# Kernel tuning notes

Hardware: AMD Instinct MI355X
Metric: run time of the kernel (lower is better)

The kernel has to match this reference:

```python
import jax, jax.numpy as jnp
import numpy as np

E = 8          # num_experts
D = 768        # d_model
H = 3072       # d_hidden
TOP_K = 2


def setup_inputs() -> dict:
    key = jax.random.key(0)
    ks = jax.random.split(key, 8)
    s_in = 1.0 / np.sqrt(D)
    s_h = 1.0 / np.sqrt(H)
    return {
        "hidden_states": jax.random.normal(ks[0], (2, 2048, D), dtype=jnp.float32),
        "gate_w": jax.random.normal(ks[1], (E, D), dtype=jnp.float32) * s_in,
        "gate_b": jnp.zeros((E,), dtype=jnp.float32),
        "w1": jax.random.normal(ks[2], (E, H, D), dtype=jnp.float32) * s_in,  # FMoELinear: [E, out, in]
        "b1": jnp.zeros((E, H), dtype=jnp.float32),
        "w2": jax.random.normal(ks[3], (E, D, H), dtype=jnp.float32) * s_h,
        "b2": jnp.zeros((E, D), dtype=jnp.float32),
        "bias": jnp.zeros((D,), dtype=jnp.float32),
    }


def reference(hidden_states, gate_w, gate_b, w1, b1, w2, b2, bias):
    B, S, d = hidden_states.shape
    x = hidden_states.reshape(-1, d)                      # [T, D]
    T = x.shape[0]
    # NaiveGate: linear gate, top-k, softmax over the top-k logits
    logits = x @ gate_w.T + gate_b                        # [T, E]
    top_val, top_idx = jax.lax.top_k(logits, TOP_K)       # [T, K]
    scores = jax.nn.softmax(top_val, axis=-1)             # [T, K]
    # combine weights: [T, E], score mass scattered to chosen experts
    combine = jnp.zeros((T, E), dtype=x.dtype)
    combine = combine.at[jnp.arange(T)[:, None], top_idx].add(scores)
    # expert MLPs (dense over experts, masked combine keeps routing math exact)
    h = jnp.einsum('td,ehd->teh', x, w1) + b1             # [T, E, H]
    h = jax.nn.gelu(h, approximate=False)                 # torch F.gelu (exact erf)
    y = jnp.einsum('teh,edh->ted', h, w2) + b2            # [T, E, D]
    out = jnp.einsum('te,ted->td', combine, y)            # [T, D]
    return out.reshape(B, S, d), bias
```

## Files before the change

### kernel.cpp

```cpp
#include <hip/hip_runtime.h>
#include <hip/hip_bf16.h>

#define DD 768
#define HH 3072
#define NE 8
#define TOPK 2

#define BK 64
#define NB1 (HH / 128)
#define NB2 (DD / 128)
#define SK2 2

typedef __attribute__((ext_vector_type(8))) short short8;
typedef __attribute__((ext_vector_type(4))) float f32x4;

static __device__ __forceinline__ unsigned short f2bf(float v) {
    __hip_bfloat16 b = __float2bfloat16(v);
    return *reinterpret_cast<unsigned short*>(&b);
}

static __device__ __forceinline__ float gelu_f(float v) {
    float s = v * 0.70710678118f;
    float a = fabsf(s);
    float t = __builtin_amdgcn_rcpf(1.f + 0.3275911f * a);
    float poly = t * (0.254829592f + t * (-0.284496736f + t * (1.421413741f +
                 t * (-1.453152027f + t * 1.061405429f))));
    float erfv = 1.f - poly * __expf(-s * s);
    erfv = copysignf(erfv, s);
    return 0.5f * v * (1.f + erfv);
}

__global__ __launch_bounds__(256) void convert_kernel(
    const float* __restrict__ w1, const float* __restrict__ w2,
    unsigned short* __restrict__ w1b, unsigned short* __restrict__ w2b, size_t n)
{
    size_t tid = (size_t)blockIdx.x * blockDim.x + threadIdx.x;
    size_t stride = (size_t)gridDim.x * blockDim.x;
    size_t quarter = n / 4;
    size_t tot = 2 * quarter;
    for (size_t j = tid; j < tot; j += stride) {
        const float* src; unsigned short* dst; size_t off;
        if (j < quarter) { src = w1; dst = w1b; off = j * 4; }
        else             { src = w2; dst = w2b; off = (j - quarter) * 4; }
        float4 v = *reinterpret_cast<const float4*>(&src[off]);
        ushort4 o;
        o.x = f2bf(v.x); o.y = f2bf(v.y); o.z = f2bf(v.z); o.w = f2bf(v.w);
        *reinterpret_cast<ushort4*>(&dst[off]) = o;
    }
}

__global__ __launch_bounds__(256) void init_kernel(int* token_map, int* ctrl, int* qcur, int maxP)
{
    int i = blockIdx.x * blockDim.x + threadIdx.x;
    if (i < maxP) token_map[i] = -1;
    if (i < 64) ctrl[i] = 0;
    if (i < 256) qcur[i] = 0;
}

__global__ __launch_bounds__(256) void gate_kernel(
    const float* __restrict__ x, const float* __restrict__ gw, const float* __restrict__ gb,
    int* __restrict__ topk_idx, float* __restrict__ topk_w, int* __restrict__ ctrl, int T)
{
    __shared__ int hist[NE];
    int tid = threadIdx.x;
    if (tid < NE) hist[tid] = 0;
    __syncthreads();

    int w = tid >> 6, lane = tid & 63;
    for (int t = blockIdx.x * 4 + w; t < T; t += gridDim.x * 4) {
        float acc[NE];
#pragma unroll
        for (int e = 0; e < NE; ++e) acc[e] = 0.f;
        const float4* xr = reinterpret_cast<const float4*>(x + (size_t)t * DD);
        for (int d = lane; d < DD / 4; d += 64) {
            float4 xv = xr[d];
#pragma unroll
            for (int e = 0; e < NE; ++e) {
                float4 gv = *reinterpret_cast<const float4*>(&gw[e * DD + 4 * d]);
                acc[e] += xv.x * gv.x + xv.y * gv.y + xv.z * gv.z + xv.w * gv.w;
            }
        }
#pragma unroll
        for (int e = 0; e < NE; ++e) {
            float v = acc[e];
            for (int off = 32; off; off >>= 1) v += __shfl_xor(v, off, 64);
            acc[e] = v;
        }
        if (lane == 0) {
            float lg[NE];
#pragma unroll
            for (int e = 0; e < NE; ++e) lg[e] = acc[e] + gb[e];
            int i0 = 0;
#pragma unroll
            for (int e = 1; e < NE; ++e) if (lg[e] > lg[i0]) i0 = e;
            int i1 = -1;
#pragma unroll
            for (int e = 0; e < NE; ++e) {
                if (e == i0) continue;
                if (i1 < 0 || lg[e] > lg[i1]) i1 = e;
            }
            float m = lg[i0];
            float e0 = __expf(lg[i0] - m), e1 = __expf(lg[i1] - m);
            float s = e0 + e1;
            topk_idx[2 * t]     = i0;
            topk_idx[2 * t + 1] = i1;
            topk_w[2 * t]       = e0 / s;
            topk_w[2 * t + 1]   = e1 / s;
            atomicAdd(&hist[i0], 1);
            atomicAdd(&hist[i1], 1);
        }
    }
    __syncthreads();
    if (tid < NE && hist[tid] > 0) atomicAdd(&ctrl[tid], hist[tid]);
}

__global__ void offsets_kernel(int* ctrl, int* wq1, int* wq2)
{
    if (threadIdx.x == 0 && blockIdx.x == 0) {
        int nrbs[NE];
        int acc = 0;
        for (int e = 0; e < NE; ++e) {
            ctrl[16 + e] = acc;
            int nrb = (ctrl[e] + 127) >> 7;
            nrbs[e] = nrb;
            acc += nrb << 7;
        }
        ctrl[24] = acc;
        int qc[8], qcum[8];
        for (int q = 0; q < 8; ++q) { qc[q] = 0; qcum[q] = 0; }
        for (int pair = 0; pair < NE * NB1; ++pair) {
            int e = pair / NB1;
            int q = pair & 7;
            int s = qc[q]++;
            qcum[q] += nrbs[e];
            wq1[(q * 24 + s) * 2 + 0] = pair;
            wq1[(q * 24 + s) * 2 + 1] = qcum[q];
        }
        for (int q = 0; q < 8; ++q) { qc[q] = 0; qcum[q] = 0; }
        for (int g = 0; g < NE * NB2 * SK2; ++g) {
            int e = g / (NB2 * SK2);
            int q = g & 7;
            int s = qc[q]++;
            qcum[q] += nrbs[e];
            wq2[(q * 12 + s) * 2 + 0] = g;
            wq2[(q * 12 + s) * 2 + 1] = qcum[q];
        }
    }
}

__global__ __launch_bounds__(256) void scatter_kernel(
    const int* __restrict__ topk_idx, const float* __restrict__ topk_w,
    int* ctrl, int* token_map, int* pos_of, float* wpos, int nA)
{
    __shared__ int lh[NE], lbase[NE];
    int tid = threadIdx.x;
    if (tid < NE) lh[tid] = 0;
    __syncthreads();

    int a = blockIdx.x * blockDim.x + tid;
    int e = 0, rank = 0;
    bool valid = (a < nA);
    if (valid) {
        e = topk_idx[a];
        rank = atomicAdd(&lh[e], 1);
    }
    __syncthreads();
    if (tid < NE && lh[tid] > 0)
        lbase[tid] = atomicAdd(&ctrl[8 + tid], lh[tid]);
    __syncthreads();
    if (valid) {
        int p = ctrl[16 + e] + lbase[e] + rank;
        token_map[p] = a;
        pos_of[a] = p;
        wpos[p] = topk_w[a];
    }
}

__global__ __launch_bounds__(256) void gather_kernel(
    const float* __restrict__ x, const int* __restrict__ token_map,
    unsigned short* __restrict__ Xe, int maxP)
{
    int i = blockIdx.x * blockDim.x + threadIdx.x;
    int total = maxP * (DD / 4);
    if (i >= total) return;
    int r = i / (DD / 4);
    int c = (i % (DD / 4)) * 4;
    int a = token_map[r];
    ushort4 o;
    if (a < 0) {
        o.x = o.y = o.z = o.w = 0;
    } else {
        float4 v = *reinterpret_cast<const float4*>(&x[(size_t)(a >> 1) * DD + c]);
        o.x = f2bf(v.x); o.y = f2bf(v.y); o.z = f2bf(v.z); o.w = f2bf(v.w);
    }
    *reinterpret_cast<ushort4*>(&Xe[(size_t)r * DD + c]) = o;
}

static __device__ __forceinline__ void stage_tile(
    const unsigned short* __restrict__ g, int ld, unsigned short* __restrict__ lds)
{
    int tid = threadIdx.x;
#pragma unroll
    for (int r = 0; r < 4; ++r) {
        int j = (r << 8) + tid;
        int row = j >> 3;
        int kc = (j & 7) ^ (row & 7);
        __builtin_amdgcn_global_load_lds(
            (const __attribute__((address_space(1))) void*)(g + (size_t)row * ld + (kc << 3)),
            (__attribute__((address_space(3))) void*)(lds + (j << 3)),
            16, 0, 0);
    }
}

#define LDSF(base, row, kc) \
    reinterpret_cast<const short8*>(&(base)[((((row) << 3) + ((kc) ^ ((row) & 7))) << 3)])

static __device__ __forceinline__ void gemm_item(
    const unsigned short* __restrict__ Abase,
    const unsigned short* __restrict__ Bbase,
    int ld, int nt,
    unsigned short* __restrict__ As, unsigned short* __restrict__ Bs,
    f32x4 acc[4][4], int wr, int wc, int fr, int fq)
{
    const int BUF = 128 * 64;
    stage_tile(Abase, ld, As);
    stage_tile(Bbase, ld, Bs);
    for (int t = 0; t < nt; ++t) {
        int cur = t & 1;
        if (t + 1 < nt) {
            stage_tile(Abase + (size_t)(t + 1) * BK, ld, As + (cur ^ 1) * BUF);
            stage_tile(Bbase + (size_t)(t + 1) * BK, ld, Bs + (cur ^ 1) * BUF);
            asm volatile("s_waitcnt vmcnt(8)" ::: "memory");
        } else {
            asm volatile("s_waitcnt vmcnt(0)" ::: "memory");
        }
        __builtin_amdgcn_s_barrier();
        asm volatile("" ::: "memory");

        const unsigned short* A = As + cur * BUF;
        const unsigned short* B = Bs + cur * BUF;
        short8 a[2][4], b[2][4];
#pragma unroll
        for (int ks = 0; ks < 2; ++ks) {
            int kc = ks * 4 + fq;
#pragma unroll
            for (int m = 0; m < 4; ++m)
                a[ks][m] = *LDSF(A, wr + m * 16 + fr, kc);
#pragma unroll
            for (int n = 0; n < 4; ++n)
                b[ks][n] = *LDSF(B, wc + n * 16 + fr, kc);
        }
        __builtin_amdgcn_s_setprio(1);
#pragma unroll
        for (int ks = 0; ks < 2; ++ks)
#pragma unroll
            for (int m = 0; m < 4; ++m)
#pragma unroll
                for (int n = 0; n < 4; ++n)
                    acc[m][n] = __builtin_amdgcn_mfma_f32_16x16x32_bf16(
                        b[ks][n], a[ks][m], acc[m][n], 0, 0, 0);
        __builtin_amdgcn_s_setprio(0);
        asm volatile("s_waitcnt lgkmcnt(0)" ::: "memory");
        __builtin_amdgcn_s_barrier();
        asm volatile("" ::: "memory");
    }
}


__global__ __launch_bounds__(256, 2) void gemm1_kernel(
    const unsigned short* __restrict__ Xe, const unsigned short* __restrict__ W1b,
    const float* __restrict__ b1, unsigned short* __restrict__ H1,
    const int* __restrict__ ctrl, const int* __restrict__ wq1, int* __restrict__ qcur)
{
    __shared__ unsigned short As[2 * 128 * 64];
    __shared__ unsigned short Bs[2 * 128 * 64];
    __shared__ int sh_item;
    __shared__ int seg[9];
    __shared__ int tpair[192], tcum[192];

    int tid = threadIdx.x;
    if (tid < 9) seg[tid] = ctrl[16 + tid];
    if (tid < 192) { tpair[tid] = wq1[2 * tid]; tcum[tid] = wq1[2 * tid + 1]; }
    __syncthreads();

    int lane = tid & 63, w = tid >> 6;
    int wr = (w >> 1) * 64, wc = (w & 1) * 64;
    int fr = lane & 15, fq = lane >> 4;
    int q0 = blockIdx.x & 7;

    for (int off = 0; off < 8; ++off) {
        int qq = (q0 + off) & 7;
        int qtot = tcum[qq * 24 + 23];
        for (;;) {
            if (tid == 0) sh_item = atomicAdd(&qcur[qq * 16], 1);
            __syncthreads();
            int j = sh_item;
            __syncthreads();
            if (j >= qtot) break;

            int s = 0;
            while (tcum[qq * 24 + s] <= j) ++s;
            int pair = tpair[qq * 24 + s];
            int start = s ? tcum[qq * 24 + s - 1] : 0;
            int rb = j - start;
            int e = pair / NB1, cb = pair - e * NB1;
            int rowbase = seg[e] + (rb << 7);
            int colbase = cb << 7;

            const unsigned short* Abase = Xe + (size_t)rowbase * DD;
            const unsigned short* Bbase = W1b + (size_t)e * HH * DD + (size_t)colbase * DD;

            f32x4 acc[4][4];
#pragma unroll
            for (int m = 0; m < 4; ++m)
#pragma unroll
                for (int n = 0; n < 4; ++n) acc[m][n] = (f32x4){0.f, 0.f, 0.f, 0.f};

            gemm_item(Abase, Bbase, DD, DD / BK, As, Bs, acc, wr, wc, fr, fq);

            float4 bb[4];
#pragma unroll
            for (int n = 0; n < 4; ++n)
                bb[n] = *reinterpret_cast<const float4*>(
                    &b1[e * HH + colbase + wc + n * 16 + fq * 4]);
#pragma unroll
            for (int m = 0; m < 4; ++m) {
                int tok = rowbase + wr + m * 16 + fr;
#pragma unroll
                for (int n = 0; n < 4; ++n) {
                    int ch = colbase + wc + n * 16 + fq * 4;
                    ushort4 o;
                    o.x = f2bf(gelu_f(acc[m][n][0] + bb[n].x));
                    o.y = f2bf(gelu_f(acc[m][n][1] + bb[n].y));
                    o.z = f2bf(gelu_f(acc[m][n][2] + bb[n].z));
                    o.w = f2bf(gelu_f(acc[m][n][3] + bb[n].w));
                    *reinterpret_cast<ushort4*>(&H1[(size_t)tok * HH + ch]) = o;
                }
            }
        }
    }
}

__global__ __launch_bounds__(256, 2) void gemm2_kernel(
    const unsigned short* __restrict__ H1, const unsigned short* __restrict__ W2b,
    const float* __restrict__ b2, const float* __restrict__ wpos,
    float* __restrict__ Yb, const int* __restrict__ ctrl,
    const int* __restrict__ wq2, int* __restrict__ qcur, int maxP)
{
    __shared__ unsigned short As[2 * 128 * 64];
    __shared__ unsigned short Bs[2 * 128 * 64];
    __shared__ int sh_item;
    __shared__ int seg[9];
    __shared__ int tpair[96], tcum[96];

    int tid = threadIdx.x;
    if (tid < 9) seg[tid] = ctrl[16 + tid];
    if (tid < 96) { tpair[tid] = wq2[2 * tid]; tcum[tid] = wq2[2 * tid + 1]; }
    __syncthreads();

    int lane = tid & 63, w = tid >> 6;
    int wr = (w >> 1) * 64, wc = (w & 1) * 64;
    int fr = lane & 15, fq = lane >> 4;
    int q0 = blockIdx.x & 7;
    size_t Ysz = (size_t)maxP * DD;

    for (int off = 0; off < 8; ++off) {
        int qq = (q0 + off) & 7;
        int qtot = tcum[qq * 12 + 11];
        for (;;) {
            if (tid == 0) sh_item = atomicAdd(&qcur[(8 + qq) * 16], 1);
            __syncthreads();
            int j = sh_item;
            __syncthreads();
            if (j >= qtot) break;

            int s = 0;
            while (tcum[qq * 12 + s] <= j) ++s;
            int g = tpair[qq * 12 + s];
            int start = s ? tcum[qq * 12 + s - 1] : 0;
            int rb = j - start;
            int e = g / (NB2 * SK2);
            int rem = g - e * (NB2 * SK2);
            int cb = rem >> 1;
            int sk = rem & 1;
            int rowbase = seg[e] + (rb << 7);
            int colbase = cb << 7;

            const unsigned short* Abase = H1 + (size_t)rowbase * HH + sk * (HH / 2);
            const unsigned short* Bbase = W2b + (size_t)e * DD * HH + (size_t)colbase * HH + sk * (HH / 2);

            f32x4 acc[4][4];
#pragma unroll
            for (int m = 0; m < 4; ++m)
#pragma unroll
                for (int n = 0; n < 4; ++n) acc[m][n] = (f32x4){0.f, 0.f, 0.f, 0.f};

            gemm_item(Abase, Bbase, HH, HH / BK / SK2, As, Bs, acc, wr, wc, fr, fq);

            float* Yp = Yb + (size_t)sk * Ysz;
            float4 bb[4];
#pragma unroll
            for (int n = 0; n < 4; ++n) {
                float4 b4 = *reinterpret_cast<const float4*>(
                    &b2[e * DD + colbase + wc + n * 16 + fq * 4]);
                bb[n].x = 0.5f * b4.x; bb[n].y = 0.5f * b4.y;
                bb[n].z = 0.5f * b4.z; bb[n].w = 0.5f * b4.w;
            }
#pragma unroll
            for (int m = 0; m < 4; ++m) {
                int tok = rowbase + wr + m * 16 + fr;
                float wp = wpos[tok];
#pragma unroll
                for (int n = 0; n < 4; ++n) {
                    int ch = colbase + wc + n * 16 + fq * 4;
                    float4 o;
                    o.x = wp * (acc[m][n][0] + bb[n].x);
                    o.y = wp * (acc[m][n][1] + bb[n].y);
                    o.z = wp * (acc[m][n][2] + bb[n].z);
                    o.w = wp * (acc[m][n][3] + bb[n].w);
                    *reinterpret_cast<float4*>(&Yp[(size_t)tok * DD + ch]) = o;
                }
            }
        }
    }
}

__global__ __launch_bounds__(256) void combine_kernel(
    const float* __restrict__ Yb, const int* __restrict__ pos_of,
    const float* __restrict__ bias, float* __restrict__ out, int T, int maxP)
{
    int i = blockIdx.x * blockDim.x + threadIdx.x;
    int total = T * (DD / 4);
    size_t Ysz = (size_t)maxP * DD;
    if (i < total) {
        int t = i / (DD / 4);
        int c = (i % (DD / 4)) * 4;
        int p0 = pos_of[2 * t], p1 = pos_of[2 * t + 1];
        float4 v00 = *reinterpret_cast<const float4*>(&Yb[(size_t)p0 * DD + c]);
        float4 v01 = *reinterpret_cast<const float4*>(&Yb[Ysz + (size_t)p0 * DD + c]);
        float4 v10 = *reinterpret_cast<const float4*>(&Yb[(size_t)p1 * DD + c]);
        float4 v11 = *reinterpret_cast<const float4*>(&Yb[Ysz + (size_t)p1 * DD + c]);
        float4 o;
        o.x = v00.x + v01.x + v10.x + v11.x;
        o.y = v00.y + v01.y + v10.y + v11.y;
        o.z = v00.z + v01.z + v10.z + v11.z;
        o.w = v00.w + v01.w + v10.w + v11.w;
        *reinterpret_cast<float4*>(&out[(size_t)t * DD + c]) = o;
    } else if (i < total + DD / 4) {
        int c = (i - total) * 4;
        *reinterpret_cast<float4*>(&out[(size_t)T * DD + c]) =
            *reinterpret_cast<const float4*>(&bias[c]);
    }
}

extern "C" void kernel_launch(void* const* d_in, const int* in_sizes, int n_in,
                              void* d_out, int out_size, void* d_ws, size_t ws_size,
                              hipStream_t stream)
{
    const float* x    = (const float*)d_in[0];
    const float* gw   = (const float*)d_in[1];
    const float* gb   = (const float*)d_in[2];
    const float* w1   = (const float*)d_in[3];
    const float* b1   = (const float*)d_in[4];
    const float* w2   = (const float*)d_in[5];
    const float* b2   = (const float*)d_in[6];
    const float* bias = (const float*)d_in[7];
    float* out = (float*)d_out;

    int T = in_sizes[0] / DD;
    int nA = T * TOPK;
    int maxP = nA + NE * 128;

    char* ws = (char*)d_ws;
    size_t off = 0;
    auto alloc = [&](size_t bytes) -> char* {
        char* p = ws + off;
        off += (bytes + 255) & ~(size_t)255;
        return p;
    };
    unsigned short* w1b = (unsigned short*)alloc((size_t)NE * HH * DD * 2);
    unsigned short* w2b = (unsigned short*)alloc((size_t)NE * DD * HH * 2);
    unsigned short* Xe  = (unsigned short*)alloc((size_t)maxP * DD * 2);
    unsigned short* H1  = (unsigned short*)alloc((size_t)maxP * HH * 2);
    float*  Yb          = (float*)alloc((size_t)SK2 * maxP * DD * 4);
    int*    topk_idx    = (int*)alloc((size_t)nA * 4);
    float*  topk_w      = (float*)alloc((size_t)nA * 4);
    int*    pos_of      = (int*)alloc((size_t)nA * 4);
    float*  wpos        = (float*)alloc((size_t)maxP * 4);
    int*    token_map   = (int*)alloc((size_t)maxP * 4);
    int*    ctrl        = (int*)alloc(64 * 4);
    int*    wq1         = (int*)alloc(384 * 4);
    int*    wq2         = (int*)alloc(192 * 4);
    int*    qcur        = (int*)alloc(256 * 4);

    size_t nW = (size_t)NE * HH * DD;

    hipLaunchKernelGGL(convert_kernel, dim3(4096), dim3(256), 0, stream,
                       w1, w2, w1b, w2b, nW);
    hipLaunchKernelGGL(init_kernel, dim3((maxP + 255) / 256), dim3(256), 0, stream,
                       token_map, ctrl, qcur, maxP);
    hipLaunchKernelGGL(gate_kernel, dim3(512), dim3(256), 0, stream,
                       x, gw, gb, topk_idx, topk_w, ctrl, T);
    hipLaunchKernelGGL(offsets_kernel, dim3(1), dim3(64), 0, stream, ctrl, wq1, wq2);
    hipLaunchKernelGGL(scatter_kernel, dim3((nA + 255) / 256), dim3(256), 0, stream,
                       topk_idx, topk_w, ctrl, token_map, pos_of, wpos, nA);
    hipLaunchKernelGGL(gather_kernel, dim3((maxP * (DD / 4) + 255) / 256), dim3(256), 0, stream,
                       x, token_map, Xe, maxP);
    hipLaunchKernelGGL(gemm1_kernel, dim3(512), dim3(256), 0, stream,
                       Xe, w1b, b1, H1, ctrl, wq1, qcur);
    hipLaunchKernelGGL(gemm2_kernel, dim3(512), dim3(256), 0, stream,
                       H1, w2b, b2, wpos, Yb, ctrl, wq2, qcur, maxP);
    hipLaunchKernelGGL(combine_kernel, dim3((T * (DD / 4) + DD / 4 + 255) / 256, 1, 1), dim3(256), 0, stream,
                       Yb, pos_of, bias, out, T, maxP);
}
```

Baseline: 254.2 us.

## Fuse routing stages into a cooperative kernel and drop split-K in expert GEMM2

The gate, offsets, scatter and gather kernels are merged into one cooperative route kernel that uses grid-wide syncs. The init kernel is folded into the weight-convert kernel, and the token_map/padding zero-fill is removed. GEMM2 no longer splits K in two, which halves the Yb buffer and lets combine read two partial rows instead of four. The aim is fewer launches and less intermediate traffic, at the cost of about half as many GEMM2 work items, lower parallelism, and padding rows of Xe left uninitialised.

```diff
diff --git a/kernel.cpp b/kernel.cpp
--- a/kernel.cpp
+++ b/kernel.cpp
@@ -1,5 +1,8 @@
 #include <hip/hip_runtime.h>
 #include <hip/hip_bf16.h>
+#include <hip/hip_cooperative_groups.h>
+
+namespace cg = cooperative_groups;
 
 #define DD 768
 #define HH 3072
@@ -9,7 +12,6 @@
 #define BK 64
 #define NB1 (HH / 128)
 #define NB2 (DD / 128)
-#define SK2 2
 
 typedef __attribute__((ext_vector_type(8))) short short8;
 typedef __attribute__((ext_vector_type(4))) float f32x4;
@@ -32,9 +34,12 @@
 
 __global__ __launch_bounds__(256) void convert_kernel(
     const float* __restrict__ w1, const float* __restrict__ w2,
-    unsigned short* __restrict__ w1b, unsigned short* __restrict__ w2b, size_t n)
+    unsigned short* __restrict__ w1b, unsigned short* __restrict__ w2b,
+    int* __restrict__ ctrl, int* __restrict__ qcur, size_t n)
 {
     size_t tid = (size_t)blockIdx.x * blockDim.x + threadIdx.x;
+    if (tid < 64) ctrl[tid] = 0;
+    if (tid < 256) qcur[tid] = 0;
     size_t stride = (size_t)gridDim.x * blockDim.x;
     size_t quarter = n / 4;
     size_t tot = 2 * quarter;
@@ -49,79 +54,78 @@
     }
 }
 
-__global__ __launch_bounds__(256) void init_kernel(int* token_map, int* ctrl, int* qcur, int maxP)
-{
-    int i = blockIdx.x * blockDim.x + threadIdx.x;
-    if (i < maxP) token_map[i] = -1;
-    if (i < 64) ctrl[i] = 0;
-    if (i < 256) qcur[i] = 0;
-}
-
-__global__ __launch_bounds__(256) void gate_kernel(
+__global__ __launch_bounds__(256) void route_kernel(
     const float* __restrict__ x, const float* __restrict__ gw, const float* __restrict__ gb,
-    int* __restrict__ topk_idx, float* __restrict__ topk_w, int* __restrict__ ctrl, int T)
-{
+    int* __restrict__ topk_idx, float* __restrict__ topk_w_unused, int* __restrict__ ctrl,
+    int* __restrict__ wq1, int* __restrict__ wq2,
+    int* __restrict__ pos_of, float* __restrict__ wpos, float* __restrict__ topk_w,
+    unsigned short* __restrict__ Xe, int T, int nA)
+{
+    cg::grid_group grid = cg::this_grid();
+    int tid = threadIdx.x, bid = blockIdx.x, nb = gridDim.x;
+    int gidx = bid * 256 + tid;
+
     __shared__ int hist[NE];
-    int tid = threadIdx.x;
     if (tid < NE) hist[tid] = 0;
     __syncthreads();
-
-    int w = tid >> 6, lane = tid & 63;
-    for (int t = blockIdx.x * 4 + w; t < T; t += gridDim.x * 4) {
-        float acc[NE];
-#pragma unroll
-        for (int e = 0; e < NE; ++e) acc[e] = 0.f;
-        const float4* xr = reinterpret_cast<const float4*>(x + (size_t)t * DD);
-        for (int d = lane; d < DD / 4; d += 64) {
-            float4 xv = xr[d];
+    {
+        int w = tid >> 6, lane = tid & 63;
+        for (int t = bid * 4 + w; t < T; t += nb * 4) {
+            float acc[NE];
+#pragma unroll
+            for (int e = 0; e < NE; ++e) acc[e] = 0.f;
+            const float4* xr = reinterpret_cast<const float4*>(x + (size_t)t * DD);
+            for (int d = lane; d < DD / 4; d += 64) {
+                float4 xv = xr[d];
+#pragma unroll
+                for (int e = 0; e < NE; ++e) {
+                    float4 gv = *reinterpret_cast<const float4*>(&gw[e * DD + 4 * d]);
+                    acc[e] += xv.x * gv.x + xv.y * gv.y + xv.z * gv.z + xv.w * gv.w;
+                }
+            }
 #pragma unroll
             for (int e = 0; e < NE; ++e) {
-                float4 gv = *reinterpret_cast<const float4*>(&gw[e * DD + 4 * d]);
-                acc[e] += xv.x * gv.x + xv.y * gv.y + xv.z * gv.z + xv.w * gv.w;
-            }
-        }
-#pragma unroll
-        for (int e = 0; e < NE; ++e) {
-            float v = acc[e];
-            for (int off = 32; off; off >>= 1) v += __shfl_xor(v, off, 64);
-            acc[e] = v;
-        }
-        if (lane == 0) {
-            float lg[NE];
-#pragma unroll
-            for (int e = 0; e < NE; ++e) lg[e] = acc[e] + gb[e];
-            int i0 = 0;
-#pragma unroll
-            for (int e = 1; e < NE; ++e) if (lg[e] > lg[i0]) i0 = e;
-            int i1 = -1;
-#pragma unroll
-            for (int e = 0; e < NE; ++e) {
-                if (e == i0) continue;
-                if (i1 < 0 || lg[e] > lg[i1]) i1 = e;
-            }
-            float m = lg[i0];
-            float e0 = __expf(lg[i0] - m), e1 = __expf(lg[i1] - m);
-            float s = e0 + e1;
-            topk_idx[2 * t]     = i0;
-            topk_idx[2 * t + 1] = i1;
-            topk_w[2 * t]       = e0 / s;
-            topk_w[2 * t + 1]   = e1 / s;
-            atomicAdd(&hist[i0], 1);
-            atomicAdd(&hist[i1], 1);
+                float v = acc[e];
+                for (int off = 32; off; off >>= 1) v += __shfl_xor(v, off, 64);
+                acc[e] = v;
+            }
+            if (lane == 0) {
+                float lg[NE];
+#pragma unroll
+                for (int e = 0; e < NE; ++e) lg[e] = acc[e] + gb[e];
+                int i0 = 0;
+#pragma unroll
+                for (int e = 1; e < NE; ++e) if (lg[e] > lg[i0]) i0 = e;
+                int i1 = -1;
+#pragma unroll
+                for (int e = 0; e < NE; ++e) {
+                    if (e == i0) continue;
+                    if (i1 < 0 || lg[e] > lg[i1]) i1 = e;
+                }
+                float m = lg[i0];
+                float e0 = __expf(lg[i0] - m), e1 = __expf(lg[i1] - m);
+                float s = e0 + e1;
+                topk_idx[2 * t]     = i0;
+                topk_idx[2 * t + 1] = i1;
+                topk_w[2 * t]       = e0 / s;
+                topk_w[2 * t + 1]   = e1 / s;
+                atomicAdd(&hist[i0], 1);
+                atomicAdd(&hist[i1], 1);
+            }
         }
     }
     __syncthreads();
     if (tid < NE && hist[tid] > 0) atomicAdd(&ctrl[tid], hist[tid]);
-}
-
-__global__ void offsets_kernel(int* ctrl, int* wq1, int* wq2)
-{
-    if (threadIdx.x == 0 && blockIdx.x == 0) {
+    __threadfence();
+    grid.sync();
+
+    if (bid == 0 && tid == 0) {
         int nrbs[NE];
         int acc = 0;
         for (int e = 0; e < NE; ++e) {
             ctrl[16 + e] = acc;
-            int nrb = (ctrl[e] + 127) >> 7;
+            int cnt = atomicAdd(&ctrl[e], 0);
+            int nrb = (cnt + 127) >> 7;
             nrbs[e] = nrb;
             acc += nrb << 7;
         }
@@ -137,63 +141,57 @@
             wq1[(q * 24 + s) * 2 + 1] = qcum[q];
         }
         for (int q = 0; q < 8; ++q) { qc[q] = 0; qcum[q] = 0; }
-        for (int g = 0; g < NE * NB2 * SK2; ++g) {
-            int e = g / (NB2 * SK2);
+        for (int g = 0; g < NE * NB2; ++g) {
+            int e = g / NB2;
             int q = g & 7;
             int s = qc[q]++;
             qcum[q] += nrbs[e];
-            wq2[(q * 12 + s) * 2 + 0] = g;
-            wq2[(q * 12 + s) * 2 + 1] = qcum[q];
-        }
-    }
-}
-
-__global__ __launch_bounds__(256) void scatter_kernel(
-    const int* __restrict__ topk_idx, const float* __restrict__ topk_w,
-    int* ctrl, int* token_map, int* pos_of, float* wpos, int nA)
-{
-    __shared__ int lh[NE], lbase[NE];
-    int tid = threadIdx.x;
-    if (tid < NE) lh[tid] = 0;
-    __syncthreads();
-
-    int a = blockIdx.x * blockDim.x + tid;
-    int e = 0, rank = 0;
-    bool valid = (a < nA);
-    if (valid) {
-        e = topk_idx[a];
-        rank = atomicAdd(&lh[e], 1);
-    }
-    __syncthreads();
-    if (tid < NE && lh[tid] > 0)
-        lbase[tid] = atomicAdd(&ctrl[8 + tid], lh[tid]);
-    __syncthreads();
-    if (valid) {
-        int p = ctrl[16 + e] + lbase[e] + rank;
-        token_map[p] = a;
-        pos_of[a] = p;
-        wpos[p] = topk_w[a];
-    }
-}
-
-__global__ __launch_bounds__(256) void gather_kernel(
-    const float* __restrict__ x, const int* __restrict__ token_map,
-    unsigned short* __restrict__ Xe, int maxP)
-{
-    int i = blockIdx.x * blockDim.x + threadIdx.x;
-    int total = maxP * (DD / 4);
-    if (i >= total) return;
-    int r = i / (DD / 4);
-    int c = (i % (DD / 4)) * 4;
-    int a = token_map[r];
-    ushort4 o;
-    if (a < 0) {
-        o.x = o.y = o.z = o.w = 0;
-    } else {
-        float4 v = *reinterpret_cast<const float4*>(&x[(size_t)(a >> 1) * DD + c]);
-        o.x = f2bf(v.x); o.y = f2bf(v.y); o.z = f2bf(v.z); o.w = f2bf(v.w);
-    }
-    *reinterpret_cast<ushort4*>(&Xe[(size_t)r * DD + c]) = o;
+            wq2[(q * 6 + s) * 2 + 0] = g;
+            wq2[(q * 6 + s) * 2 + 1] = qcum[q];
+        }
+        __threadfence();
+    }
+    grid.sync();
+
+    {
+        __shared__ int lh[NE], lbase[NE];
+        for (int a0 = 0; a0 < nA; a0 += nb * 256) {
+            if (tid < NE) lh[tid] = 0;
+            __syncthreads();
+            int a = a0 + gidx;
+            int e = 0, rank = 0;
+            bool valid = (a < nA);
+            if (valid) {
+                e = topk_idx[a];
+                rank = atomicAdd(&lh[e], 1);
+            }
+            __syncthreads();
+            if (tid < NE && lh[tid] > 0)
+                lbase[tid] = atomicAdd(&ctrl[8 + tid], lh[tid]);
+            __syncthreads();
+            if (valid) {
+                int p = ctrl[16 + e] + lbase[e] + rank;
+                pos_of[a] = p;
+                wpos[p] = topk_w[a];
+            }
+            __syncthreads();
+        }
+    }
+    __threadfence();
+    grid.sync();
+
+    {
+        int tot = nA * (DD / 4);
+        for (int i = gidx; i < tot; i += nb * 256) {
+            int a = i / (DD / 4);
+            int c = (i % (DD / 4)) * 4;
+            int p = pos_of[a];
+            float4 v = *reinterpret_cast<const float4*>(&x[(size_t)(a >> 1) * DD + c]);
+            ushort4 o;
+            o.x = f2bf(v.x); o.y = f2bf(v.y); o.z = f2bf(v.z); o.w = f2bf(v.w);
+            *reinterpret_cast<ushort4*>(&Xe[(size_t)p * DD + c]) = o;
+        }
+    }
 }
 
 static __device__ __forceinline__ void stage_tile(
@@ -345,28 +343,27 @@
     const unsigned short* __restrict__ H1, const unsigned short* __restrict__ W2b,
     const float* __restrict__ b2, const float* __restrict__ wpos,
     float* __restrict__ Yb, const int* __restrict__ ctrl,
-    const int* __restrict__ wq2, int* __restrict__ qcur, int maxP)
+    const int* __restrict__ wq2, int* __restrict__ qcur)
 {
     __shared__ unsigned short As[2 * 128 * 64];
     __shared__ unsigned short Bs[2 * 128 * 64];
     __shared__ int sh_item;
     __shared__ int seg[9];
-    __shared__ int tpair[96], tcum[96];
+    __shared__ int tpair[48], tcum[48];
 
     int tid = threadIdx.x;
     if (tid < 9) seg[tid] = ctrl[16 + tid];
-    if (tid < 96) { tpair[tid] = wq2[2 * tid]; tcum[tid] = wq2[2 * tid + 1]; }
+    if (tid < 48) { tpair[tid] = wq2[2 * tid]; tcum[tid] = wq2[2 * tid + 1]; }
     __syncthreads();
 
     int lane = tid & 63, w = tid >> 6;
     int wr = (w >> 1) * 64, wc = (w & 1) * 64;
     int fr = lane & 15, fq = lane >> 4;
     int q0 = blockIdx.x & 7;
-    size_t Ysz = (size_t)maxP * DD;
 
     for (int off = 0; off < 8; ++off) {
         int qq = (q0 + off) & 7;
-        int qtot = tcum[qq * 12 + 11];
+        int qtot = tcum[qq * 6 + 5];
         for (;;) {
             if (tid == 0) sh_item = atomicAdd(&qcur[(8 + qq) * 16], 1);
             __syncthreads();
@@ -375,19 +372,16 @@
             if (j >= qtot) break;
 
             int s = 0;
-            while (tcum[qq * 12 + s] <= j) ++s;
-            int g = tpair[qq * 12 + s];
-            int start = s ? tcum[qq * 12 + s - 1] : 0;
+            while (tcum[qq * 6 + s] <= j) ++s;
+            int g = tpair[qq * 6 + s];
+            int start = s ? tcum[qq * 6 + s - 1] : 0;
             int rb = j - start;
-            int e = g / (NB2 * SK2);
-            int rem = g - e * (NB2 * SK2);
-            int cb = rem >> 1;
-            int sk = rem & 1;
+            int e = g / NB2, cb = g - e * NB2;
             int rowbase = seg[e] + (rb << 7);
             int colbase = cb << 7;
 
-            const unsigned short* Abase = H1 + (size_t)rowbase * HH + sk * (HH / 2);
-            const unsigned short* Bbase = W2b + (size_t)e * DD * HH + (size_t)colbase * HH + sk * (HH / 2);
+            const unsigned short* Abase = H1 + (size_t)rowbase * HH;
+            const unsigned short* Bbase = W2b + (size_t)e * DD * HH + (size_t)colbase * HH;
 
             f32x4 acc[4][4];
 #pragma unroll
@@ -395,17 +389,13 @@
 #pragma unroll
                 for (int n = 0; n < 4; ++n) acc[m][n] = (f32x4){0.f, 0.f, 0.f, 0.f};
 
-            gemm_item(Abase, Bbase, HH, HH / BK / SK2, As, Bs, acc, wr, wc, fr, fq);
-
-            float* Yp = Yb + (size_t)sk * Ysz;
+            gemm_item(Abase, Bbase, HH, HH / BK, As, Bs, acc, wr, wc, fr, fq);
+
             float4 bb[4];
 #pragma unroll
-            for (int n = 0; n < 4; ++n) {
-                float4 b4 = *reinterpret_cast<const float4*>(
+            for (int n = 0; n < 4; ++n)
+                bb[n] = *reinterpret_cast<const float4*>(
                     &b2[e * DD + colbase + wc + n * 16 + fq * 4]);
-                bb[n].x = 0.5f * b4.x; bb[n].y = 0.5f * b4.y;
-                bb[n].z = 0.5f * b4.z; bb[n].w = 0.5f * b4.w;
-            }
 #pragma unroll
             for (int m = 0; m < 4; ++m) {
                 int tok = rowbase + wr + m * 16 + fr;
@@ -418,7 +408,7 @@
                     o.y = wp * (acc[m][n][1] + bb[n].y);
                     o.z = wp * (acc[m][n][2] + bb[n].z);
                     o.w = wp * (acc[m][n][3] + bb[n].w);
-                    *reinterpret_cast<float4*>(&Yp[(size_t)tok * DD + ch]) = o;
+                    *reinterpret_cast<float4*>(&Yb[(size_t)tok * DD + ch]) = o;
                 }
             }
         }
@@ -427,24 +417,19 @@
 
 __global__ __launch_bounds__(256) void combine_kernel(
     const float* __restrict__ Yb, const int* __restrict__ pos_of,
-    const float* __restrict__ bias, float* __restrict__ out, int T, int maxP)
+    const float* __restrict__ bias, float* __restrict__ out, int T)
 {
     int i = blockIdx.x * blockDim.x + threadIdx.x;
     int total = T * (DD / 4);
-    size_t Ysz = (size_t)maxP * DD;
     if (i < total) {
         int t = i / (DD / 4);
         int c = (i % (DD / 4)) * 4;
         int p0 = pos_of[2 * t], p1 = pos_of[2 * t + 1];
-        float4 v00 = *reinterpret_cast<const float4*>(&Yb[(size_t)p0 * DD + c]);
-        float4 v01 = *reinterpret_cast<const float4*>(&Yb[Ysz + (size_t)p0 * DD + c]);
-        float4 v10 = *reinterpret_cast<const float4*>(&Yb[(size_t)p1 * DD + c]);
-        float4 v11 = *reinterpret_cast<const float4*>(&Yb[Ysz + (size_t)p1 * DD + c]);
+        float4 v0 = *reinterpret_cast<const float4*>(&Yb[(size_t)p0 * DD + c]);
+        float4 v1 = *reinterpret_cast<const float4*>(&Yb[(size_t)p1 * DD + c]);
         float4 o;
-        o.x = v00.x + v01.x + v10.x + v11.x;
-        o.y = v00.y + v01.y + v10.y + v11.y;
-        o.z = v00.z + v01.z + v10.z + v11.z;
-        o.w = v00.w + v01.w + v10.w + v11.w;
+        o.x = v0.x + v1.x; o.y = v0.y + v1.y;
+        o.z = v0.z + v1.z; o.w = v0.w + v1.w;
         *reinterpret_cast<float4*>(&out[(size_t)t * DD + c]) = o;
     } else if (i < total + DD / 4) {
         int c = (i - total) * 4;
@@ -482,34 +467,37 @@
     unsigned short* w2b = (unsigned short*)alloc((size_t)NE * DD * HH * 2);
     unsigned short* Xe  = (unsigned short*)alloc((size_t)maxP * DD * 2);
     unsigned short* H1  = (unsigned short*)alloc((size_t)maxP * HH * 2);
-    float*  Yb          = (float*)alloc((size_t)SK2 * maxP * DD * 4);
+    float*  Yb          = (float*)alloc((size_t)maxP * DD * 4);
     int*    topk_idx    = (int*)alloc((size_t)nA * 4);
     float*  topk_w      = (float*)alloc((size_t)nA * 4);
     int*    pos_of      = (int*)alloc((size_t)nA * 4);
     float*  wpos        = (float*)alloc((size_t)maxP * 4);
-    int*    token_map   = (int*)alloc((size_t)maxP * 4);
     int*    ctrl        = (int*)alloc(64 * 4);
     int*    wq1         = (int*)alloc(384 * 4);
-    int*    wq2         = (int*)alloc(192 * 4);
+    int*    wq2         = (int*)alloc(96 * 4);
     int*    qcur        = (int*)alloc(256 * 4);
 
     size_t nW = (size_t)NE * HH * DD;
 
     hipLaunchKernelGGL(convert_kernel, dim3(4096), dim3(256), 0, stream,
-                       w1, w2, w1b, w2b, nW);
-    hipLaunchKernelGGL(init_kernel, dim3((maxP + 255) / 256), dim3(256), 0, stream,
-                       token_map, ctrl, qcur, maxP);
-    hipLaunchKernelGGL(gate_kernel, dim3(512), dim3(256), 0, stream,
-                       x, gw, gb, topk_idx, topk_w, ctrl, T);
-    hipLaunchKernelGGL(offsets_kernel, dim3(1), dim3(64), 0, stream, ctrl, wq1, wq2);
-    hipLaunchKernelGGL(scatter_kernel, dim3((nA + 255) / 256), dim3(256), 0, stream,
-                       topk_idx, topk_w, ctrl, token_map, pos_of, wpos, nA);
-    hipLaunchKernelGGL(gather_kernel, dim3((maxP * (DD / 4) + 255) / 256), dim3(256), 0, stream,
-                       x, token_map, Xe, maxP);
+                       w1, w2, w1b, w2b, ctrl, qcur, nW);
+
+    {
+        const float* xa = x; const float* gwa = gw; const float* gba = gb;
+        int* ti = topk_idx; float* twu = topk_w; int* ct = ctrl;
+        int* q1 = wq1; int* q2 = wq2;
+        int* po = pos_of; float* wp = wpos; float* tw = topk_w;
+        unsigned short* xe = Xe; int Ta = T; int nAa = nA;
+        void* args[] = { &xa, &gwa, &gba, &ti, &twu, &ct, &q1, &q2,
+                         &po, &wp, &tw, &xe, &Ta, &nAa };
+        hipLaunchCooperativeKernel((const void*)route_kernel,
+                                   dim3(256), dim3(256), args, 0, stream);
+    }
+
     hipLaunchKernelGGL(gemm1_kernel, dim3(512), dim3(256), 0, stream,
                        Xe, w1b, b1, H1, ctrl, wq1, qcur);
     hipLaunchKernelGGL(gemm2_kernel, dim3(512), dim3(256), 0, stream,
-                       H1, w2b, b2, wpos, Yb, ctrl, wq2, qcur, maxP);
+                       H1, w2b, b2, wpos, Yb, ctrl, wq2, qcur);
     hipLaunchKernelGGL(combine_kernel, dim3((T * (DD / 4) + DD / 4 + 255) / 256, 1, 1), dim3(256), 0, stream,
-                       Yb, pos_of, bias, out, T, maxP);
-}
+                       Yb, pos_of, bias, out, T);
+}
```

New measurement: 350.4 us. 1.38x slower.
